# Kernel optimization log

Measured on AMD Instinct MI355X. Metric: run time of the kernel, lower is better.

## Reference

```python
import jax, jax.numpy as jnp
import numpy as np

S, H, A = 16384, 1024, 1024


def setup_inputs() -> dict:
    key = jax.random.key(0)
    k1, k2, k3, k4, k5, k6 = jax.random.split(key, 6)
    enc_out = jax.random.normal(k1, (S, 1, H), dtype=jnp.float32)
    dec_h = jax.random.normal(k2, (1, H), dtype=jnp.float32)
    mask = jax.random.randint(k3, (S, 1), 0, 2) == 1  # bool [S,1]
    # learned params (torch Linear stores weight as [out, in]; y = x @ W.T)
    W2_dec = jax.random.normal(k4, (A, H), dtype=jnp.float32) * 0.02
    W1_enc = jax.random.normal(k5, (A, H), dtype=jnp.float32) * 0.02
    V = jax.random.normal(k6, (1, A), dtype=jnp.float32) * 0.02
    return {"enc_out": enc_out, "dec_h": dec_h, "mask": mask,
            "W2_dec": W2_dec, "W1_enc": W1_enc, "V": V}


def reference(enc_out, dec_h, mask, W2_dec, W1_enc, V):
    enc = jnp.squeeze(enc_out, axis=1)            # [S, H]
    d = dec_h @ W2_dec.T                          # [1, A]
    e = enc @ W1_enc.T                            # [S, A]
    u = jnp.tanh(d + e) @ V.T                     # [S, 1]
    u = jnp.where(mask, -jnp.inf, u)              # masked logits (returned, like in-place fill)
    a = jax.nn.softmax(u, axis=0)                 # softmax over seq dim
    out = jnp.sum(a * enc, axis=0)                # [H]
    return (out, u)
```

## Files before the change

kernel.cpp:

```cpp
#include <hip/hip_runtime.h>
#include <math.h>
#include <stdint.h>

#define S_DIM 16384
#define H_DIM 1024
#define A_DIM 1024

#define MASK_NEG (-3.0e38f)

typedef __attribute__((ext_vector_type(8))) _Float16 f16x8;
typedef __attribute__((ext_vector_type(4))) float f32x4;
typedef __attribute__((address_space(3))) uint32_t as3_u32;
typedef __attribute__((address_space(1))) uint32_t as1_u32;

__global__ __launch_bounds__(256) void prep_kernel(
        const float* __restrict__ enc, _Float16* __restrict__ enc_h,
        const float* __restrict__ W1, _Float16* __restrict__ W1_h,
        const float* __restrict__ dec_h, const float* __restrict__ W2,
        float* __restrict__ d, float* __restrict__ u_acc) {
    const int b = blockIdx.x;
    const int t = threadIdx.x;
    if (b < 8704) {
        const float* src = (b < 8192) ? enc : W1;
        _Float16* dst    = (b < 8192) ? enc_h : W1_h;
        const int i = ((b < 8192) ? b : (b - 8192)) * 256 + t;
        float4 v0 = ((const float4*)src)[2 * i];
        float4 v1 = ((const float4*)src)[2 * i + 1];
        union { _Float16 h[8]; uint4 u; } pk;
        pk.h[0] = (_Float16)v0.x; pk.h[1] = (_Float16)v0.y;
        pk.h[2] = (_Float16)v0.z; pk.h[3] = (_Float16)v0.w;
        pk.h[4] = (_Float16)v1.x; pk.h[5] = (_Float16)v1.y;
        pk.h[6] = (_Float16)v1.z; pk.h[7] = (_Float16)v1.w;
        ((uint4*)dst)[i] = pk.u;
        if (b < 64) u_acc[b * 256 + t] = 0.0f;
    } else {
        const int a = b - 8704;
        const float* row = W2 + (size_t)a * H_DIM;
        float s = 0.0f;
        for (int h = t; h < H_DIM; h += 256) s += dec_h[h] * row[h];
        #pragma unroll
        for (int off = 32; off; off >>= 1) s += __shfl_down(s, off, 64);
        __shared__ float wsum[4];
        if ((t & 63) == 0) wsum[t >> 6] = s;
        __syncthreads();
        if (t == 0) d[a] = wsum[0] + wsum[1] + wsum[2] + wsum[3];
    }
}

__global__ __launch_bounds__(256) void fused_gemm_f16(
        const _Float16* __restrict__ Ag,
        const _Float16* __restrict__ Bg,
        const float* __restrict__ V,
        const float* __restrict__ d,
        float* __restrict__ u_acc) {
    __shared__ _Float16 At[128 * 64];
    __shared__ _Float16 Bt[128 * 64];
    __shared__ float P[128][2];

    const int tid  = threadIdx.x;
    const int wave = tid >> 6;
    const int lane = tid & 63;
    const int quad = lane >> 4;
    const int l16  = lane & 15;
    const int wm   = wave >> 1;
    const int wn   = wave & 1;
    const int s0   = blockIdx.x * 128;
    const int a0   = blockIdx.y * 128;

    const _Float16* gsrc = (wave < 2) ? Ag : Bg;
    _Float16* tile       = (wave < 2) ? At : Bt;
    const int rbase      = (wave < 2) ? s0 : a0;
    const int rowoff     = (wave & 1) * 64;
    const int lrow = lane >> 3;
    const int lchk = lane & 7;
    const int cg   = (lchk + lrow) & 7;

    f32x4 acc[4][4];
    #pragma unroll
    for (int mi = 0; mi < 4; ++mi)
        #pragma unroll
        for (int ni = 0; ni < 4; ++ni)
            acc[mi][ni] = (f32x4){0.f, 0.f, 0.f, 0.f};

    for (int kt = 0; kt < H_DIM / 64; ++kt) {
        const _Float16* g0 = gsrc + (size_t)(rbase + rowoff + lrow) * H_DIM
                             + kt * 64 + cg * 8;
        #pragma unroll
        for (int j = 0; j < 8; ++j) {
            __builtin_amdgcn_global_load_lds(
                (const as1_u32*)(const void*)(g0 + (size_t)j * 8 * H_DIM),
                (as3_u32*)(void*)(tile + (rowoff + j * 8) * 64),
                16, 0, 0);
        }
        __syncthreads();

        #pragma unroll
        for (int ksub = 0; ksub < 2; ++ksub) {
            const int c = ksub * 4 + quad;
            f16x8 bf[4];
            #pragma unroll
            for (int ni = 0; ni < 4; ++ni) {
                int R = wn * 64 + ni * 16 + l16;
                bf[ni] = *(const f16x8*)&Bt[R * 64 + ((c - R) & 7) * 8];
            }
            #pragma unroll
            for (int mi = 0; mi < 4; ++mi) {
                int R = wm * 64 + mi * 16 + l16;
                f16x8 af = *(const f16x8*)&At[R * 64 + ((c - R) & 7) * 8];
                #pragma unroll
                for (int ni = 0; ni < 4; ++ni)
                    acc[mi][ni] = __builtin_amdgcn_mfma_f32_16x16x32_f16(af, bf[ni], acc[mi][ni], 0, 0, 0);
            }
        }
        __syncthreads();
    }

    float vv[4], dd[4];
    #pragma unroll
    for (int ni = 0; ni < 4; ++ni) {
        int c = a0 + wn * 64 + ni * 16 + l16;
        vv[ni] = V[c];
        dd[ni] = d[c];
    }
    #pragma unroll
    for (int mi = 0; mi < 4; ++mi) {
        #pragma unroll
        for (int reg = 0; reg < 4; ++reg) {
            float s = 0.0f;
            #pragma unroll
            for (int ni = 0; ni < 4; ++ni)
                s += vv[ni] * tanhf(dd[ni] + acc[mi][ni][reg]);
            #pragma unroll
            for (int off = 1; off < 16; off <<= 1)
                s += __shfl_xor(s, off, 64);
            if (l16 == 0)
                P[wm * 64 + mi * 16 + quad * 4 + reg][wn] = s;
        }
    }
    __syncthreads();
    if (tid < 128)
        atomicAdd(u_acc + s0 + tid, P[tid][0] + P[tid][1]);
}

__global__ __launch_bounds__(256) void fused_gemm(const float* __restrict__ enc,
                                                  const float* __restrict__ W1,
                                                  const float* __restrict__ V,
                                                  const float* __restrict__ d,
                                                  float* __restrict__ u_acc) {
    __shared__ __align__(16) float As[16][128 + 4];
    __shared__ __align__(16) float Bs[16][128 + 4];
    const int tid = threadIdx.x;
    const int tx = tid & 15, ty = tid >> 4;
    const int s0 = blockIdx.y * 128, a0 = blockIdx.x * 128;
    const int lr = tid >> 2, lc = tid & 3;
    float acc[8][8] = {};
    for (int kt = 0; kt < H_DIM / 16; ++kt) {
        const int k0 = kt * 16;
        float4 av0 = *(const float4*)(enc + (size_t)(s0 + lr)      * H_DIM + k0 + 4 * lc);
        float4 av1 = *(const float4*)(enc + (size_t)(s0 + lr + 64) * H_DIM + k0 + 4 * lc);
        float4 bv0 = *(const float4*)(W1  + (size_t)(a0 + lr)      * H_DIM + k0 + 4 * lc);
        float4 bv1 = *(const float4*)(W1  + (size_t)(a0 + lr + 64) * H_DIM + k0 + 4 * lc);
        __syncthreads();
        As[4*lc+0][lr] = av0.x; As[4*lc+1][lr] = av0.y; As[4*lc+2][lr] = av0.z; As[4*lc+3][lr] = av0.w;
        As[4*lc+0][lr+64] = av1.x; As[4*lc+1][lr+64] = av1.y; As[4*lc+2][lr+64] = av1.z; As[4*lc+3][lr+64] = av1.w;
        Bs[4*lc+0][lr] = bv0.x; Bs[4*lc+1][lr] = bv0.y; Bs[4*lc+2][lr] = bv0.z; Bs[4*lc+3][lr] = bv0.w;
        Bs[4*lc+0][lr+64] = bv1.x; Bs[4*lc+1][lr+64] = bv1.y; Bs[4*lc+2][lr+64] = bv1.z; Bs[4*lc+3][lr+64] = bv1.w;
        __syncthreads();
        #pragma unroll
        for (int k = 0; k < 16; ++k) {
            float4 A0 = *(const float4*)&As[k][8 * ty];
            float4 A1 = *(const float4*)&As[k][8 * ty + 4];
            float4 B0 = *(const float4*)&Bs[k][8 * tx];
            float4 B1 = *(const float4*)&Bs[k][8 * tx + 4];
            float ar[8] = {A0.x, A0.y, A0.z, A0.w, A1.x, A1.y, A1.z, A1.w};
            float br[8] = {B0.x, B0.y, B0.z, B0.w, B1.x, B1.y, B1.z, B1.w};
            #pragma unroll
            for (int i = 0; i < 8; ++i)
                #pragma unroll
                for (int j = 0; j < 8; ++j)
                    acc[i][j] = fmaf(ar[i], br[j], acc[i][j]);
        }
    }
    float vv[8], dd[8];
    #pragma unroll
    for (int j = 0; j < 8; ++j) { int c = a0 + 8 * tx + j; vv[j] = V[c]; dd[j] = d[c]; }
    float pu[8];
    #pragma unroll
    for (int i = 0; i < 8; ++i) {
        float s = 0.0f;
        #pragma unroll
        for (int j = 0; j < 8; ++j) s += vv[j] * tanhf(dd[j] + acc[i][j]);
        pu[i] = s;
    }
    __syncthreads();
    float* Pf = &As[0][0];
    #pragma unroll
    for (int i = 0; i < 8; ++i) Pf[(8 * ty + i) * 16 + tx] = pu[i];
    __syncthreads();
    if (tid < 128) {
        float s = 0.0f;
        #pragma unroll
        for (int j = 0; j < 16; ++j) s += Pf[tid * 16 + j];
        atomicAdd(u_acc + s0 + tid, s);
    }
}

__global__ __launch_bounds__(1024) void softmax_kernel(const float* __restrict__ u_acc,
                                                       const void* __restrict__ mask,
                                                       float* __restrict__ u_out,
                                                       float* __restrict__ p) {
    const int t = threadIdx.x;
    const unsigned char* mb = (const unsigned char*)mask;
    const int* mi = (const int*)mask;

    unsigned int orv = 0;
    for (int i = t; i < S_DIM; i += 1024)
        if (i & 3) orv |= mb[i];
    __shared__ int sflag;
    if (t == 0) sflag = 0;
    __syncthreads();
    if (orv) sflag = 1;
    __syncthreads();
    const int bytemask = sflag;

    float v[16];
    float lmax = -INFINITY;
    #pragma unroll
    for (int i = 0; i < 16; ++i) {
        int r = t + i * 1024;
        int m = bytemask ? (int)mb[r] : mi[r];
        float val = m ? MASK_NEG : u_acc[r];
        u_out[r] = val;
        v[i] = val;
        lmax = fmaxf(lmax, val);
    }

    __shared__ float red[16];
    __shared__ float sm, sdenom;
    #pragma unroll
    for (int off = 32; off; off >>= 1) lmax = fmaxf(lmax, __shfl_down(lmax, off, 64));
    int wid = t >> 6, lane = t & 63;
    if (lane == 0) red[wid] = lmax;
    __syncthreads();
    if (t == 0) {
        float m2 = -INFINITY;
        for (int i = 0; i < 16; ++i) m2 = fmaxf(m2, red[i]);
        sm = m2;
    }
    __syncthreads();
    const float m = sm;

    float lsum = 0.0f;
    #pragma unroll
    for (int i = 0; i < 16; ++i) {
        v[i] = expf(v[i] - m);
        lsum += v[i];
    }
    #pragma unroll
    for (int off = 32; off; off >>= 1) lsum += __shfl_down(lsum, off, 64);
    if (lane == 0) red[wid] = lsum;
    __syncthreads();
    if (t == 0) {
        float s2 = 0.0f;
        for (int i = 0; i < 16; ++i) s2 += red[i];
        sdenom = s2;
    }
    __syncthreads();
    const float inv = 1.0f / sdenom;
    #pragma unroll
    for (int i = 0; i < 16; ++i) p[t + i * 1024] = v[i] * inv;
}

__global__ __launch_bounds__(256) void wsum_part(const _Float16* __restrict__ enc_h,
                                                 const float* __restrict__ p,
                                                 float* __restrict__ part) {
    const int t = threadIdx.x;
    const int b = blockIdx.x;
    float4 acc = {0.f, 0.f, 0.f, 0.f};
    const int s0 = b * 32;
    for (int s = s0; s < s0 + 32; ++s) {
        float ps = p[s];
        union { _Float16 h[4]; uint2 u; } e;
        e.u = ((const uint2*)(enc_h + (size_t)s * H_DIM))[t];
        acc.x += ps * (float)e.h[0];
        acc.y += ps * (float)e.h[1];
        acc.z += ps * (float)e.h[2];
        acc.w += ps * (float)e.h[3];
    }
    ((float4*)(part + (size_t)b * 1024))[t] = acc;
}
__global__ __launch_bounds__(256) void wsum_reduce(const float* __restrict__ part,
                                                   float* __restrict__ out) {
    __shared__ float red[256];
    const int t = threadIdx.x;
    const int col = blockIdx.x * 16 + (t & 15);
    const int seg = t >> 4;
    float s = 0.0f;
    for (int b = seg * 32; b < seg * 32 + 32; ++b)
        s += part[(size_t)b * 1024 + col];
    red[t] = s;
    __syncthreads();
    if (t < 16) {
        float r = 0.0f;
        #pragma unroll
        for (int k = 0; k < 16; ++k) r += red[k * 16 + t];
        out[col] = r;
    }
}
__global__ __launch_bounds__(256) void weighted_sum(const float* __restrict__ enc,
                                                    const float* __restrict__ p,
                                                    float* __restrict__ out) {
    const int t = threadIdx.x;
    const int s0 = blockIdx.x * 32;
    const float4* encv = (const float4*)enc;
    float4 acc = {0.0f, 0.0f, 0.0f, 0.0f};
    for (int s = s0; s < s0 + 32; ++s) {
        float ps = p[s];
        float4 e = encv[(size_t)s * 256 + t];
        acc.x += ps * e.x; acc.y += ps * e.y; acc.z += ps * e.z; acc.w += ps * e.w;
    }
    atomicAdd(out + 4 * t + 0, acc.x);
    atomicAdd(out + 4 * t + 1, acc.y);
    atomicAdd(out + 4 * t + 2, acc.z);
    atomicAdd(out + 4 * t + 3, acc.w);
}
__global__ void zero_kernel(float* __restrict__ u_acc, float* __restrict__ out) {
    int i = blockIdx.x * 256 + threadIdx.x;
    if (i < S_DIM) u_acc[i] = 0.0f;
    if (i < H_DIM) out[i]   = 0.0f;
}
__global__ __launch_bounds__(256) void dec_proj(const float* __restrict__ dec_h,
                                                const float* __restrict__ W2,
                                                float* __restrict__ d) {
    int a = blockIdx.x;
    int t = threadIdx.x;
    const float* row = W2 + (size_t)a * H_DIM;
    float s = 0.0f;
    for (int h = t; h < H_DIM; h += 256) s += dec_h[h] * row[h];
    #pragma unroll
    for (int off = 32; off; off >>= 1) s += __shfl_down(s, off, 64);
    __shared__ float wsum[4];
    if ((t & 63) == 0) wsum[t >> 6] = s;
    __syncthreads();
    if (t == 0) d[a] = wsum[0] + wsum[1] + wsum[2] + wsum[3];
}

extern "C" void kernel_launch(void* const* d_in, const int* in_sizes, int n_in,
                              void* d_out, int out_size, void* d_ws, size_t ws_size,
                              hipStream_t stream) {
    const float* enc   = (const float*)d_in[0];
    const float* dec_h = (const float*)d_in[1];
    const void*  mask  = d_in[2];
    const float* W2    = (const float*)d_in[3];
    const float* W1    = (const float*)d_in[4];
    const float* V     = (const float*)d_in[5];

    float* out   = (float*)d_out;
    float* u_out = (float*)d_out + H_DIM;

    float* ws    = (float*)d_ws;
    float* d     = ws;
    float* u_acc = ws + A_DIM;
    float* p     = ws + A_DIM + S_DIM;
    float* part  = ws + A_DIM + 2 * S_DIM;
    size_t f_end = (size_t)(A_DIM + 2 * S_DIM + 512 * 1024);
    _Float16* enc_h = (_Float16*)(ws + f_end);
    _Float16* W1_h  = enc_h + (size_t)S_DIM * H_DIM;
    size_t need_bytes = f_end * 4
                      + (size_t)S_DIM * H_DIM * 2
                      + (size_t)A_DIM * H_DIM * 2;

    if (ws_size >= need_bytes) {
        prep_kernel<<<9728, 256, 0, stream>>>(enc, enc_h, W1, W1_h,
                                              dec_h, W2, d, u_acc);
        fused_gemm_f16<<<dim3(S_DIM / 128, A_DIM / 128), 256, 0, stream>>>(
            enc_h, W1_h, V, d, u_acc);
        softmax_kernel<<<1, 1024, 0, stream>>>(u_acc, mask, u_out, p);
        wsum_part<<<S_DIM / 32, 256, 0, stream>>>(enc_h, p, part);
        wsum_reduce<<<64, 256, 0, stream>>>(part, out);
    } else {
        zero_kernel<<<64, 256, 0, stream>>>(u_acc, out);
        dec_proj<<<A_DIM, 256, 0, stream>>>(dec_h, W2, d);
        fused_gemm<<<dim3(A_DIM / 128, S_DIM / 128), 256, 0, stream>>>(enc, W1, V, d, u_acc);
        softmax_kernel<<<1, 1024, 0, stream>>>(u_acc, mask, u_out, p);
        weighted_sum<<<S_DIM / 32, 256, 0, stream>>>(enc, p, out);
    }
}
```

Measured before the change: 197.7 us.

## Double-buffer GEMM LDS tiles with K=32 stages to overlap loads and MFMA

Splits the 128x64 K-tile into two 128x32 LDS buffers and issues the async global-to-LDS loads for the next K stage before running MFMAs on the current one. The aim is to hide global load latency behind compute rather than stalling on a sync before every tile. The LDS swizzle and precomputed fragment offsets are rewritten for the narrower 32-wide rows. Total LDS stays the same, but the kernel now has one barrier per K=32 step and relies on the ping-pong ordering being correct.

New measurement: 203.7 us. 3.0% more time.

```diff
diff --git a/kernel.cpp b/kernel.cpp
--- a/kernel.cpp
+++ b/kernel.cpp
@@ -53,8 +53,8 @@
         const float* __restrict__ V,
         const float* __restrict__ d,
         float* __restrict__ u_acc) {
-    __shared__ _Float16 At[128 * 64];
-    __shared__ _Float16 Bt[128 * 64];
+    __shared__ _Float16 At[2][128 * 32];
+    __shared__ _Float16 Bt[2][128 * 32];
     __shared__ float P[128][2];
 
     const int tid  = threadIdx.x;
@@ -68,12 +68,25 @@
     const int a0   = blockIdx.y * 128;
 
     const _Float16* gsrc = (wave < 2) ? Ag : Bg;
-    _Float16* tile       = (wave < 2) ? At : Bt;
+    _Float16* tbase      = (wave < 2) ? &At[0][0] : &Bt[0][0];
     const int rbase      = (wave < 2) ? s0 : a0;
     const int rowoff     = (wave & 1) * 64;
-    const int lrow = lane >> 3;
-    const int lchk = lane & 7;
-    const int cg   = (lchk + lrow) & 7;
+    const int lrow = lane >> 2;
+    const int cg   = ((lane & 3) + (lrow >> 1)) & 3;
+
+    const _Float16* grow[4];
+    #pragma unroll
+    for (int j = 0; j < 4; ++j)
+        grow[j] = gsrc + (size_t)(rbase + rowoff + j * 16 + lrow) * H_DIM + cg * 8;
+    _Float16* lrow0 = tbase + rowoff * 32;
+
+    const int sw = ((quad - (l16 >> 1)) & 3) * 8;
+    int aoff[4], boff[4];
+    #pragma unroll
+    for (int f = 0; f < 4; ++f) {
+        aoff[f] = (wm * 64 + f * 16 + l16) * 32 + sw;
+        boff[f] = (wn * 64 + f * 16 + l16) * 32 + sw;
+    }
 
     f32x4 acc[4][4];
     #pragma unroll
@@ -82,31 +95,51 @@
         for (int ni = 0; ni < 4; ++ni)
             acc[mi][ni] = (f32x4){0.f, 0.f, 0.f, 0.f};
 
-    for (int kt = 0; kt < H_DIM / 64; ++kt) {
-        const _Float16* g0 = gsrc + (size_t)(rbase + rowoff + lrow) * H_DIM
-                             + kt * 64 + cg * 8;
-        #pragma unroll
-        for (int j = 0; j < 8; ++j) {
+    {
+        #pragma unroll
+        for (int j = 0; j < 4; ++j)
             __builtin_amdgcn_global_load_lds(
-                (const as1_u32*)(const void*)(g0 + (size_t)j * 8 * H_DIM),
-                (as3_u32*)(void*)(tile + (rowoff + j * 8) * 64),
-                16, 0, 0);
+                (const as1_u32*)(const void*)(grow[j]),
+                (as3_u32*)(void*)(lrow0 + j * 512), 16, 0, 0);
+    }
+    __syncthreads();
+
+    for (int kt = 0; kt < H_DIM / 32; kt += 2) {
+        {
+            #pragma unroll
+            for (int j = 0; j < 4; ++j)
+                __builtin_amdgcn_global_load_lds(
+                    (const as1_u32*)(const void*)(grow[j] + (kt + 1) * 32),
+                    (as3_u32*)(void*)(lrow0 + 4096 + j * 512), 16, 0, 0);
+        }
+        {
+            f16x8 bf[4];
+            #pragma unroll
+            for (int ni = 0; ni < 4; ++ni) bf[ni] = *(const f16x8*)&Bt[0][boff[ni]];
+            #pragma unroll
+            for (int mi = 0; mi < 4; ++mi) {
+                f16x8 af = *(const f16x8*)&At[0][aoff[mi]];
+                #pragma unroll
+                for (int ni = 0; ni < 4; ++ni)
+                    acc[mi][ni] = __builtin_amdgcn_mfma_f32_16x16x32_f16(af, bf[ni], acc[mi][ni], 0, 0, 0);
+            }
         }
         __syncthreads();
 
-        #pragma unroll
-        for (int ksub = 0; ksub < 2; ++ksub) {
-            const int c = ksub * 4 + quad;
+        if (kt + 2 < H_DIM / 32) {
+            #pragma unroll
+            for (int j = 0; j < 4; ++j)
+                __builtin_amdgcn_global_load_lds(
+                    (const as1_u32*)(const void*)(grow[j] + (kt + 2) * 32),
+                    (as3_u32*)(void*)(lrow0 + j * 512), 16, 0, 0);
+        }
+        {
             f16x8 bf[4];
             #pragma unroll
-            for (int ni = 0; ni < 4; ++ni) {
-                int R = wn * 64 + ni * 16 + l16;
-                bf[ni] = *(const f16x8*)&Bt[R * 64 + ((c - R) & 7) * 8];
-            }
+            for (int ni = 0; ni < 4; ++ni) bf[ni] = *(const f16x8*)&Bt[1][boff[ni]];
             #pragma unroll
             for (int mi = 0; mi < 4; ++mi) {
-                int R = wm * 64 + mi * 16 + l16;
-                f16x8 af = *(const f16x8*)&At[R * 64 + ((c - R) & 7) * 8];
+                f16x8 af = *(const f16x8*)&At[1][aoff[mi]];
                 #pragma unroll
                 for (int ni = 0; ni < 4; ++ni)
                     acc[mi][ni] = __builtin_amdgcn_mfma_f32_16x16x32_f16(af, bf[ni], acc[mi][ni], 0, 0, 0);
```

## Load MFMA operands directly from global memory instead of staging through LDS

Applied to the files above, without the earlier changes.

Removes the shared-memory tiles and global_load_lds staging in the fused GEMM. Each wave now reads its f16x8 A and B fragments straight from global memory in a fully unrolled K loop, and the block barriers go away. Launch bounds are raised to request 3 blocks per CU to help hide latency. The cost is that operands shared between waves are no longer reused from LDS, so the same data is fetched several times from global memory or L2 with narrow per-lane row reads, and the full unroll raises register pressure.

Result: slower. 259.7 us (+31.4%).

```diff
diff --git a/kernel.cpp b/kernel.cpp
--- a/kernel.cpp
+++ b/kernel.cpp
@@ -10,8 +10,6 @@
 
 typedef __attribute__((ext_vector_type(8))) _Float16 f16x8;
 typedef __attribute__((ext_vector_type(4))) float f32x4;
-typedef __attribute__((address_space(3))) uint32_t as3_u32;
-typedef __attribute__((address_space(1))) uint32_t as1_u32;
 
 __global__ __launch_bounds__(256) void prep_kernel(
         const float* __restrict__ enc, _Float16* __restrict__ enc_h,
@@ -47,14 +45,12 @@
     }
 }
 
-__global__ __launch_bounds__(256) void fused_gemm_f16(
+__global__ __launch_bounds__(256, 3) void fused_gemm_f16(
         const _Float16* __restrict__ Ag,
         const _Float16* __restrict__ Bg,
         const float* __restrict__ V,
         const float* __restrict__ d,
         float* __restrict__ u_acc) {
-    __shared__ _Float16 At[128 * 64];
-    __shared__ _Float16 Bt[128 * 64];
     __shared__ float P[128][2];
 
     const int tid  = threadIdx.x;
@@ -67,13 +63,14 @@
     const int s0   = blockIdx.x * 128;
     const int a0   = blockIdx.y * 128;
 
-    const _Float16* gsrc = (wave < 2) ? Ag : Bg;
-    _Float16* tile       = (wave < 2) ? At : Bt;
-    const int rbase      = (wave < 2) ? s0 : a0;
-    const int rowoff     = (wave & 1) * 64;
-    const int lrow = lane >> 3;
-    const int lchk = lane & 7;
-    const int cg   = (lchk + lrow) & 7;
+    const _Float16* arow[4];
+    const _Float16* brow[4];
+    #pragma unroll
+    for (int mi = 0; mi < 4; ++mi)
+        arow[mi] = Ag + (size_t)(s0 + wm * 64 + mi * 16 + l16) * H_DIM + quad * 8;
+    #pragma unroll
+    for (int ni = 0; ni < 4; ++ni)
+        brow[ni] = Bg + (size_t)(a0 + wn * 64 + ni * 16 + l16) * H_DIM + quad * 8;
 
     f32x4 acc[4][4];
     #pragma unroll
@@ -82,37 +79,21 @@
         for (int ni = 0; ni < 4; ++ni)
             acc[mi][ni] = (f32x4){0.f, 0.f, 0.f, 0.f};
 
-    for (int kt = 0; kt < H_DIM / 64; ++kt) {
-        const _Float16* g0 = gsrc + (size_t)(rbase + rowoff + lrow) * H_DIM
-                             + kt * 64 + cg * 8;
-        #pragma unroll
-        for (int j = 0; j < 8; ++j) {
-            __builtin_amdgcn_global_load_lds(
-                (const as1_u32*)(const void*)(g0 + (size_t)j * 8 * H_DIM),
-                (as3_u32*)(void*)(tile + (rowoff + j * 8) * 64),
-                16, 0, 0);
-        }
-        __syncthreads();
-
-        #pragma unroll
-        for (int ksub = 0; ksub < 2; ++ksub) {
-            const int c = ksub * 4 + quad;
-            f16x8 bf[4];
+    #pragma unroll
+    for (int kt = 0; kt < H_DIM / 32; ++kt) {
+        f16x8 af[4], bf[4];
+        #pragma unroll
+        for (int mi = 0; mi < 4; ++mi)
+            af[mi] = *(const f16x8*)(arow[mi] + kt * 32);
+        #pragma unroll
+        for (int ni = 0; ni < 4; ++ni)
+            bf[ni] = *(const f16x8*)(brow[ni] + kt * 32);
+        #pragma unroll
+        for (int mi = 0; mi < 4; ++mi)
             #pragma unroll
-            for (int ni = 0; ni < 4; ++ni) {
-                int R = wn * 64 + ni * 16 + l16;
-                bf[ni] = *(const f16x8*)&Bt[R * 64 + ((c - R) & 7) * 8];
-            }
-            #pragma unroll
-            for (int mi = 0; mi < 4; ++mi) {
-                int R = wm * 64 + mi * 16 + l16;
-                f16x8 af = *(const f16x8*)&At[R * 64 + ((c - R) & 7) * 8];
-                #pragma unroll
-                for (int ni = 0; ni < 4; ++ni)
-                    acc[mi][ni] = __builtin_amdgcn_mfma_f32_16x16x32_f16(af, bf[ni], acc[mi][ni], 0, 0, 0);
-            }
-        }
-        __syncthreads();
+            for (int ni = 0; ni < 4; ++ni)
+                acc[mi][ni] = __builtin_amdgcn_mfma_f32_16x16x32_f16(
+                    af[mi], bf[ni], acc[mi][ni], 0, 0, 0);
     }
 
     float vv[4], dd[4];
```
